# Performance work log

Hardware: AMD Instinct MI355X
Metric: run time of the kernel (lower is better)

The kernel has to match this reference:

```python
import jax, jax.numpy as jnp
import numpy as np

VOC_SIZE = 65536
DIM = 256
BATCH = 4096
NUM_TOPK = 32
TEMPERATURE = 1.0


def setup_inputs() -> dict:
    key = jax.random.key(0)
    ks = jax.random.split(key, 8)
    scale = 1.0 / np.sqrt(DIM)
    return {
        "x": jax.random.normal(ks[0], (BATCH, DIM), dtype=jnp.float32),
        "codebook": jax.random.normal(ks[1], (VOC_SIZE, DIM), dtype=jnp.float32),
        "Wq": jax.random.normal(ks[2], (DIM, DIM), dtype=jnp.float32) * scale,
        "bq": jax.random.normal(ks[3], (DIM,), dtype=jnp.float32) * scale,
        "Wk": jax.random.normal(ks[4], (DIM, DIM), dtype=jnp.float32) * scale,
        "bk": jax.random.normal(ks[5], (DIM,), dtype=jnp.float32) * scale,
        "Wv": jax.random.normal(ks[6], (DIM, DIM), dtype=jnp.float32) * scale,
        "bv": jax.random.normal(ks[7], (DIM,), dtype=jnp.float32) * scale,
    }


def reference(x, codebook, Wq, bq, Wk, bk, Wv, bv):
    # Linear projections (torch Linear: y = x @ W.T + b)
    q = x @ Wq.T + bq                      # [B, D]
    k = codebook @ Wk.T + bk               # [V, D]
    v = codebook @ Wv.T + bv               # [V, D]

    dots = jnp.einsum('bd,kd->bk', q, k)   # [B, V]
    top_value, top_ind = jax.lax.top_k(dots, NUM_TOPK)  # sorted desc, like torch.topk

    # mask everything strictly below the k-th largest score
    vk = top_value[:, -1:]                 # [B, 1]
    mask_value = -jnp.finfo(dots.dtype).max
    dots_masked = jnp.where(dots < vk, mask_value, dots)

    attn = jax.nn.softmax(dots_masked / TEMPERATURE, axis=-1)
    out = jnp.einsum('bk,kd->bd', attn, v)  # [B, D]
    return (out, top_value, top_ind, dots_masked)
```

## Files before the change

kernel.cpp:

```cpp
#include <hip/hip_runtime.h>
#include <float.h>
#include <math.h>

#define DIMK 256
#define VOC 65536
#define BATCH 4096
#define NTOP 32

#define MASKV -3.3895313892515355e+38f

typedef __bf16 bf16x8 __attribute__((ext_vector_type(8)));
typedef float f32x4 __attribute__((ext_vector_type(4)));
typedef float f4 __attribute__((ext_vector_type(4)));
typedef unsigned int u32x4 __attribute__((ext_vector_type(4)));
typedef unsigned int u32x2 __attribute__((ext_vector_type(2)));

__device__ __forceinline__ ushort f2bf(float f) {
    unsigned u = __float_as_uint(f);
    u = (u + 0x7fffu + ((u >> 16) & 1u)) >> 16;
    return (ushort)u;
}
__device__ __forceinline__ float bflo(unsigned u) { return __uint_as_float(u << 16); }
__device__ __forceinline__ float bfhi(unsigned u) { return __uint_as_float(u & 0xFFFF0000u); }

#define GLOAD_LDS16(gsrc, ldst)                                                \
    __builtin_amdgcn_global_load_lds(                                          \
        (const __attribute__((address_space(1))) unsigned int*)(gsrc),         \
        (__attribute__((address_space(3))) unsigned int*)(ldst), 16, 0, 0)

__global__ __launch_bounds__(256) void gemm_nt(
    const float* __restrict__ A, const float* __restrict__ B,
    const float* __restrict__ bias, float* __restrict__ C, int N, int swap, int obf16)
{
    __shared__ float As[16][132];
    __shared__ float Bs[16][132];
    const int bn = swap ? blockIdx.y : blockIdx.x;
    const int bm = swap ? blockIdx.x : blockIdx.y;
    const int tid = threadIdx.x;
    const int tx = tid & 15, ty = tid >> 4;
    const float* Ab = A + (size_t)bm * 128 * DIMK;
    const float* Bb = B + (size_t)bn * 128 * DIMK;

    float acc[2][2][4][4];
#pragma unroll
    for (int rg = 0; rg < 2; rg++)
#pragma unroll
        for (int cg = 0; cg < 2; cg++)
#pragma unroll
            for (int r = 0; r < 4; r++)
#pragma unroll
                for (int c = 0; c < 4; c++) acc[rg][cg][r][c] = 0.f;

    for (int k0 = 0; k0 < DIMK; k0 += 16) {
#pragma unroll
        for (int r = 0; r < 2; ++r) {
            int i = tid + r * 256;
            int row = i >> 2;
            int kc = (i & 3) << 2;
            const float4 va = *(const float4*)(Ab + (size_t)row * DIMK + k0 + kc);
            As[kc + 0][row] = va.x; As[kc + 1][row] = va.y;
            As[kc + 2][row] = va.z; As[kc + 3][row] = va.w;
            const float4 vb = *(const float4*)(Bb + (size_t)row * DIMK + k0 + kc);
            Bs[kc + 0][row] = vb.x; Bs[kc + 1][row] = vb.y;
            Bs[kc + 2][row] = vb.z; Bs[kc + 3][row] = vb.w;
        }
        __syncthreads();
#pragma unroll
        for (int k = 0; k < 16; ++k) {
            const float4 a0 = *(const float4*)&As[k][ty * 4];
            const float4 a1 = *(const float4*)&As[k][64 + ty * 4];
            const float4 b0 = *(const float4*)&Bs[k][tx * 4];
            const float4 b1 = *(const float4*)&Bs[k][64 + tx * 4];
            const float ar[2][4] = { {a0.x, a0.y, a0.z, a0.w}, {a1.x, a1.y, a1.z, a1.w} };
            const float bc[2][4] = { {b0.x, b0.y, b0.z, b0.w}, {b1.x, b1.y, b1.z, b1.w} };
#pragma unroll
            for (int rg = 0; rg < 2; rg++)
#pragma unroll
                for (int cg = 0; cg < 2; cg++)
#pragma unroll
                    for (int r = 0; r < 4; r++)
#pragma unroll
                        for (int c = 0; c < 4; c++)
                            acc[rg][cg][r][c] = fmaf(ar[rg][r], bc[cg][c], acc[rg][cg][r][c]);
        }
        __syncthreads();
    }

#pragma unroll
    for (int rg = 0; rg < 2; rg++)
#pragma unroll
        for (int r = 0; r < 4; r++) {
            size_t row = (size_t)bm * 128 + rg * 64 + ty * 4 + r;
#pragma unroll
            for (int cg = 0; cg < 2; cg++) {
                int col = bn * 128 + cg * 64 + tx * 4;
                float4 o;
                o.x = acc[rg][cg][r][0]; o.y = acc[rg][cg][r][1];
                o.z = acc[rg][cg][r][2]; o.w = acc[rg][cg][r][3];
                if (bias) {
                    o.x += bias[col + 0]; o.y += bias[col + 1];
                    o.z += bias[col + 2]; o.w += bias[col + 3];
                }
                if (obf16) {
                    ushort4 ob;
                    ob.x = f2bf(o.x); ob.y = f2bf(o.y);
                    ob.z = f2bf(o.z); ob.w = f2bf(o.w);
                    *(ushort4*)((ushort*)C + row * (size_t)N + col) = ob;
                } else {
                    *(float4*)(C + row * (size_t)N + col) = o;
                }
            }
        }
}

__global__ __launch_bounds__(256) void cast_f32_bf16(
    const float* __restrict__ src, ushort* __restrict__ dst, int n8)
{
    const int i = blockIdx.x * 256 + threadIdx.x;
    if (i >= n8) return;
    const f4 a = *(const f4*)(src + (size_t)i * 8);
    const f4 b = *(const f4*)(src + (size_t)i * 8 + 4);
    u32x4 o;
    o.x = (unsigned)f2bf(a.x) | ((unsigned)f2bf(a.y) << 16);
    o.y = (unsigned)f2bf(a.z) | ((unsigned)f2bf(a.w) << 16);
    o.z = (unsigned)f2bf(b.x) | ((unsigned)f2bf(b.y) << 16);
    o.w = (unsigned)f2bf(b.z) | ((unsigned)f2bf(b.w) << 16);
    *(u32x4*)(dst + (size_t)i * 8) = o;
}

__global__ __launch_bounds__(256) void gemm_bf16_nt(
    const ushort* __restrict__ Ab16, const ushort* __restrict__ Bb16,
    const float* __restrict__ bias, ushort* __restrict__ C, int ldc)
{
    __shared__ __align__(16) ushort As[2][128 * 32];
    __shared__ __align__(16) ushort Bs[2][128 * 32];
    const int bm = blockIdx.x;
    const int bn = blockIdx.y;
    const int tid = threadIdx.x;
    const int w = tid >> 6, l = tid & 63;
    const int wm = w >> 1, wn = w & 1;

    const ushort* Ab = Ab16 + (size_t)bm * 128 * DIMK;
    const ushort* Bb = Bb16 + (size_t)bn * 128 * DIMK;

    const int sr = l >> 2;
    const int sc = (l & 3) ^ ((l >> 3) & 3);
    const int fr = l & 15;
    const int pc = (l >> 4) ^ ((fr >> 1) & 3);

    const int slab0 = w * 2, slab1 = w * 2 + 1;
    const ushort* gA0 = Ab + (size_t)(slab0 * 16 + sr) * DIMK + sc * 8;
    const ushort* gA1 = Ab + (size_t)(slab1 * 16 + sr) * DIMK + sc * 8;
    const ushort* gB0 = Bb + (size_t)(slab0 * 16 + sr) * DIMK + sc * 8;
    const ushort* gB1 = Bb + (size_t)(slab1 * 16 + sr) * DIMK + sc * 8;

#define STAGE_G(buf, kk) do {                                    \
        GLOAD_LDS16(gA0 + (kk), &As[buf][slab0 * 512]);          \
        GLOAD_LDS16(gB0 + (kk), &Bs[buf][slab0 * 512]);          \
        GLOAD_LDS16(gA1 + (kk), &As[buf][slab1 * 512]);          \
        GLOAD_LDS16(gB1 + (kk), &Bs[buf][slab1 * 512]);          \
    } while (0)

    f32x4 acc[4][4];
    const f32x4 zero = {0.f, 0.f, 0.f, 0.f};
#pragma unroll
    for (int i = 0; i < 4; ++i)
#pragma unroll
        for (int j = 0; j < 4; ++j) acc[i][j] = zero;

    STAGE_G(0, 0);
    asm volatile("s_waitcnt vmcnt(0)" ::: "memory");
    __builtin_amdgcn_s_barrier();
    asm volatile("" ::: "memory");

#pragma unroll
    for (int t = 0; t < 8; ++t) {
        const int cur = t & 1;
        if (t < 7) STAGE_G(cur ^ 1, (t + 1) * 32);

        uint4 a4[4], b4[4];
#pragma unroll
        for (int f = 0; f < 4; ++f) {
            a4[f] = *(const uint4*)(&As[cur][(wm * 64 + f * 16 + fr) * 32 + pc * 8]);
            b4[f] = *(const uint4*)(&Bs[cur][(wn * 64 + f * 16 + fr) * 32 + pc * 8]);
        }
#pragma unroll
        for (int i = 0; i < 4; ++i)
#pragma unroll
            for (int j = 0; j < 4; ++j)
                acc[i][j] = __builtin_amdgcn_mfma_f32_16x16x32_bf16(
                    __builtin_bit_cast(bf16x8, b4[i]),
                    __builtin_bit_cast(bf16x8, a4[j]),
                    acc[i][j], 0, 0, 0);

        if (t < 7) {
            asm volatile("s_waitcnt vmcnt(0)" ::: "memory");
            __builtin_amdgcn_s_barrier();
            asm volatile("" ::: "memory");
        }
    }
#undef STAGE_G

    const int nq = (l >> 4) * 4;
    const int mc = l & 15;
#pragma unroll
    for (int i = 0; i < 4; ++i)
#pragma unroll
        for (int j = 0; j < 4; ++j) {
            const int n0 = bn * 128 + wn * 64 + i * 16 + nq;
            const size_t m = (size_t)(bm * 128 + wm * 64 + j * 16 + mc);
            const f4 bb = *(const f4*)(bias + n0);
            const float c0 = acc[i][j][0] + bb.x, c1 = acc[i][j][1] + bb.y;
            const float c2 = acc[i][j][2] + bb.z, c3 = acc[i][j][3] + bb.w;
            unsigned p0, p1;
            asm("v_cvt_pk_bf16_f32 %0, %1, %2" : "=v"(p0) : "v"(c0), "v"(c1));
            asm("v_cvt_pk_bf16_f32 %0, %1, %2" : "=v"(p1) : "v"(c2), "v"(c3));
            u32x2 pv; pv.x = p0; pv.y = p1;
            *(u32x2*)(C + m * (size_t)ldc + n0) = pv;
        }
}

__global__ __launch_bounds__(256) void dots_mfma(
    const ushort* __restrict__ Qb,
    const ushort* __restrict__ Kb,
    ushort* __restrict__ Db,
    float* __restrict__ Rm)
{
    __shared__ __align__(16) ushort As[2][128 * 32];
    __shared__ __align__(16) ushort Bs[2][128 * 32];
    const int bm = blockIdx.x;
    const int bn = blockIdx.y;
    const int tid = threadIdx.x;
    const int w = tid >> 6, l = tid & 63;
    const int wm = w >> 1, wn = w & 1;

    const ushort* Ab = Qb + (size_t)bm * 128 * DIMK;
    const ushort* Bb = Kb + (size_t)bn * 128 * DIMK;

    const int sr = l >> 2;
    const int sc = (l & 3) ^ ((l >> 3) & 3);
    const int fr = l & 15;
    const int pc = (l >> 4) ^ ((fr >> 1) & 3);

    const int slab0 = w * 2, slab1 = w * 2 + 1;
    const ushort* gA0 = Ab + (size_t)(slab0 * 16 + sr) * DIMK + sc * 8;
    const ushort* gA1 = Ab + (size_t)(slab1 * 16 + sr) * DIMK + sc * 8;
    const ushort* gB0 = Bb + (size_t)(slab0 * 16 + sr) * DIMK + sc * 8;
    const ushort* gB1 = Bb + (size_t)(slab1 * 16 + sr) * DIMK + sc * 8;

#define STAGE_DM(buf, kk) do {                                   \
        GLOAD_LDS16(gA0 + (kk), &As[buf][slab0 * 512]);          \
        GLOAD_LDS16(gB0 + (kk), &Bs[buf][slab0 * 512]);          \
        GLOAD_LDS16(gA1 + (kk), &As[buf][slab1 * 512]);          \
        GLOAD_LDS16(gB1 + (kk), &Bs[buf][slab1 * 512]);          \
    } while (0)

    f32x4 acc[4][4];
    const f32x4 zero = {0.f, 0.f, 0.f, 0.f};
#pragma unroll
    for (int i = 0; i < 4; ++i)
#pragma unroll
        for (int j = 0; j < 4; ++j) acc[i][j] = zero;

    STAGE_DM(0, 0);
    asm volatile("s_waitcnt vmcnt(0)" ::: "memory");
    __builtin_amdgcn_s_barrier();
    asm volatile("" ::: "memory");

#pragma unroll
    for (int t = 0; t < 8; ++t) {
        const int cur = t & 1;
        if (t < 7) STAGE_DM(cur ^ 1, (t + 1) * 32);

        uint4 a4[4], b4[4];
#pragma unroll
        for (int f = 0; f < 4; ++f) {
            a4[f] = *(const uint4*)(&As[cur][(wm * 64 + f * 16 + fr) * 32 + pc * 8]);
            b4[f] = *(const uint4*)(&Bs[cur][(wn * 64 + f * 16 + fr) * 32 + pc * 8]);
        }
#pragma unroll
        for (int i = 0; i < 4; ++i)
#pragma unroll
            for (int j = 0; j < 4; ++j)
                acc[i][j] = __builtin_amdgcn_mfma_f32_16x16x32_bf16(
                    __builtin_bit_cast(bf16x8, b4[i]),
                    __builtin_bit_cast(bf16x8, a4[j]),
                    acc[i][j], 0, 0, 0);

        if (t < 7) {
            asm volatile("s_waitcnt vmcnt(0)" ::: "memory");
            __builtin_amdgcn_s_barrier();
            asm volatile("" ::: "memory");
        }
    }
#undef STAGE_DM

    const int kq = (l >> 4) * 4;
    const int qc = l & 15;
#pragma unroll
    for (int i = 0; i < 4; ++i)
#pragma unroll
        for (int j = 0; j < 4; ++j) {
            const size_t q = (size_t)(bm * 128 + wm * 64 + j * 16 + qc);
            const size_t k = (size_t)(bn * 128 + wn * 64 + i * 16 + kq);
            unsigned p0, p1;
            asm("v_cvt_pk_bf16_f32 %0, %1, %2" : "=v"(p0) : "v"(acc[i][j][0]), "v"(acc[i][j][1]));
            asm("v_cvt_pk_bf16_f32 %0, %1, %2" : "=v"(p1) : "v"(acc[i][j][2]), "v"(acc[i][j][3]));
            u32x2 pv; pv.x = p0; pv.y = p1;
            *(u32x2*)(Db + q * (size_t)(2 * VOC) + k) = pv;
        }

#pragma unroll
    for (int j = 0; j < 4; ++j) {
        float m = -FLT_MAX;
#pragma unroll
        for (int i = 0; i < 4; ++i)
#pragma unroll
            for (int r = 0; r < 4; ++r) m = fmaxf(m, acc[i][j][r]);
        m = fmaxf(m, __shfl_xor(m, 16));
        m = fmaxf(m, __shfl_xor(m, 32));
        if (l < 16) {
            const size_t qrow = (size_t)(bm * 128 + wm * 64 + j * 16 + l);
            Rm[qrow * 1024 + (bn * 2 + wn)] = bflo((unsigned)f2bf(m));
        }
    }
}

__device__ __forceinline__ bool pair_gt(float av, int ai, float bv, int bi) {
    return (av > bv) || (av == bv && ai < bi);
}

__global__ __launch_bounds__(256) void row_tail(
    float* __restrict__ dots, const float* __restrict__ Rm,
    float* __restrict__ topv, int* __restrict__ topi,
    const float* __restrict__ codebook, const float* __restrict__ Wv,
    const float* __restrict__ bvec, float* __restrict__ out)
{
    const int row = blockIdx.x;
    const int tid = threadIdx.x;
    const int w = tid >> 6, l = tid & 63;
    float* rp = dots + ((size_t)row << 16);

    __shared__ float s_wt[4];
    __shared__ int   s_cnt;
    __shared__ float cv[1024];
    __shared__ int   ci[1024];
    __shared__ float s_t32v[NTOP];
    __shared__ int   s_t32i[NTOP];
    __shared__ float s_attn[NTOP];
    __shared__ float s_inv;
    __shared__ float s_wc[256];

    const f4 rv = *(const f4*)(Rm + (size_t)row * 1024 + tid * 4);
    const float tmax = fmaxf(fmaxf(rv.x, rv.y), fmaxf(rv.z, rv.w));

    float cur = tmax, Tw = -FLT_MAX;
#pragma unroll
    for (int r = 0; r < 8; ++r) {
        float m = cur;
#pragma unroll
        for (int off = 32; off; off >>= 1) m = fmaxf(m, __shfl_xor(m, off));
        Tw = m;
        cur = (cur == m) ? -FLT_MAX : cur;
    }
    if (l == 0) s_wt[w] = Tw;
    if (tid == 0) s_cnt = 0;
    __syncthreads();
    const float Tb = fminf(fminf(s_wt[0], s_wt[1]), fminf(s_wt[2], s_wt[3]));

    const u32x4* rb = (const u32x4*)rp;
#pragma unroll
    for (int c = 0; c < 4; ++c) {
        if (rv[c] >= Tb) {
            const int kt = tid * 4 + c;
#pragma unroll
            for (int g = 0; g < 8; ++g) {
                const u32x4 u = rb[kt * 8 + g];
                const float vv[8] = { bflo(u.x), bfhi(u.x), bflo(u.y), bfhi(u.y),
                                      bflo(u.z), bfhi(u.z), bflo(u.w), bfhi(u.w) };
#pragma unroll
                for (int j = 0; j < 8; ++j) {
                    if (vv[j] >= Tb) {
                        const int p = atomicAdd(&s_cnt, 1);
                        if (p < 1024) { cv[p] = vv[j]; ci[p] = kt * 64 + g * 8 + j; }
                    }
                }
            }
        }
    }
    __syncthreads();
    const int n = (s_cnt < 1024) ? s_cnt : 1024;

    if (w == 0) {
        for (int r = 0; r < NTOP; ++r) {
            float bv_ = -FLT_MAX; int bi_ = 0x7fffffff;
            for (int p = l; p < n; p += 64) {
                const float vv = cv[p]; const int ii = ci[p];
                if (pair_gt(vv, ii, bv_, bi_)) { bv_ = vv; bi_ = ii; }
            }
#pragma unroll
            for (int off = 32; off; off >>= 1) {
                const float ov = __shfl_xor(bv_, off);
                const int   oi = __shfl_xor(bi_, off);
                if (pair_gt(ov, oi, bv_, bi_)) { bv_ = ov; bi_ = oi; }
            }
            if (l == 0) {
                topv[(size_t)row * NTOP + r] = bv_;
                topi[(size_t)row * NTOP + r] = bi_;
                s_t32v[r] = bv_; s_t32i[r] = bi_;
            }
            for (int p = l; p < n; p += 64)
                if (ci[p] == bi_) { cv[p] = -FLT_MAX; ci[p] = 0x7fffffff; }
        }
    }

    {
        const f4 mv4 = { MASKV, MASKV, MASKV, MASKV };
        f4* rp4 = (f4*)rp;
        const int base = w * (VOC / 4 / 4);
        for (int c4 = base + l; c4 < base + VOC / 4 / 4; c4 += 64)
            __builtin_nontemporal_store(mv4, rp4 + c4);
    }
    __syncthreads();
    if (tid < NTOP) rp[s_t32i[tid]] = s_t32v[tid];

    if (tid < NTOP) s_attn[tid] = expf(s_t32v[tid] - s_t32v[0]);
    __syncthreads();
    if (tid == 0) {
        float s = 0.f;
        for (int j = 0; j < NTOP; j++) s += s_attn[j];
        s_inv = 1.0f / s;
    }
    __syncthreads();

    float wc = 0.f;
    for (int j = 0; j < NTOP; j++)
        wc = fmaf(s_attn[j], codebook[(size_t)s_t32i[j] * DIMK + tid], wc);
    wc *= s_inv;

    s_wc[tid] = wc;
    __syncthreads();

    float acc = bvec[tid];
    const float4* wr = (const float4*)(Wv + (size_t)tid * DIMK);
#pragma unroll 4
    for (int e = 0; e < DIMK / 4; e++) {
        float4 wv4 = wr[e];
        acc = fmaf(wv4.x, s_wc[4 * e + 0], acc);
        acc = fmaf(wv4.y, s_wc[4 * e + 1], acc);
        acc = fmaf(wv4.z, s_wc[4 * e + 2], acc);
        acc = fmaf(wv4.w, s_wc[4 * e + 3], acc);
    }
    out[(size_t)row * DIMK + tid] = acc;
}

extern "C" void kernel_launch(void* const* d_in, const int* in_sizes, int n_in,
                              void* d_out, int out_size, void* d_ws, size_t ws_size,
                              hipStream_t stream) {
    const float* x        = (const float*)d_in[0];
    const float* codebook = (const float*)d_in[1];
    const float* Wq       = (const float*)d_in[2];
    const float* bq       = (const float*)d_in[3];
    const float* Wk       = (const float*)d_in[4];
    const float* bk       = (const float*)d_in[5];
    const float* Wv       = (const float*)d_in[6];
    const float* bv       = (const float*)d_in[7];

    float* out_f = (float*)d_out;
    float* topv  = out_f + (size_t)BATCH * DIMK;
    int*   topi  = (int*)(topv + (size_t)BATCH * NTOP);
    float* dotsm = (float*)(topi + (size_t)BATCH * NTOP);

    ushort* kb16 = (ushort*)d_ws;
    ushort* qb16 = kb16 + (size_t)VOC * DIMK;
    float*  Rm   = (float*)(qb16 + (size_t)BATCH * DIMK);

    ushort* cb16  = (ushort*)dotsm;
    ushort* wkb16 = cb16 + (size_t)VOC * DIMK;

    cast_f32_bf16<<<VOC * DIMK / 8 / 256, 256, 0, stream>>>(codebook, cb16, VOC * DIMK / 8);
    cast_f32_bf16<<<DIMK * DIMK / 8 / 256, 256, 0, stream>>>(Wk, wkb16, DIMK * DIMK / 8);
    gemm_nt<<<dim3(DIMK / 128, BATCH / 128), 256, 0, stream>>>(x, Wq, bq, (float*)qb16, DIMK, 0, 1);
    gemm_bf16_nt<<<dim3(VOC / 128, DIMK / 128), 256, 0, stream>>>(cb16, wkb16, bk, kb16, DIMK);
    dots_mfma<<<dim3(BATCH / 128, VOC / 128), 256, 0, stream>>>(qb16, kb16, (ushort*)dotsm, Rm);
    row_tail<<<BATCH, 256, 0, stream>>>(dotsm, Rm, topv, topi, codebook, Wv, bv, out_f);
}
```

Baseline: 1.619 ms.

## Split row tail into select, grid-wide mask fill, and attention kernels

Breaks the per-row tail kernel into three launches. The first scans the bf16 dots and selects the top-k per row, the second does a grid-strided nontemporal fill of the whole masked dots buffer, and the third writes back the top-k values and computes the attention output. Previously the fill ran inside the same block as the serial single-wave top-k selection, so the other waves idled and the store bandwidth was tied to row scheduling. The split costs two extra launches and an extra round trip of topv/topi through global memory.

```diff
diff --git a/kernel.cpp b/kernel.cpp
--- a/kernel.cpp
+++ b/kernel.cpp
@@ -330,26 +330,18 @@
     return (av > bv) || (av == bv && ai < bi);
 }
 
-__global__ __launch_bounds__(256) void row_tail(
-    float* __restrict__ dots, const float* __restrict__ Rm,
-    float* __restrict__ topv, int* __restrict__ topi,
-    const float* __restrict__ codebook, const float* __restrict__ Wv,
-    const float* __restrict__ bvec, float* __restrict__ out)
+__global__ __launch_bounds__(256) void scan_select(
+    const float* __restrict__ dots, const float* __restrict__ Rm,
+    float* __restrict__ topv, int* __restrict__ topi)
 {
     const int row = blockIdx.x;
     const int tid = threadIdx.x;
     const int w = tid >> 6, l = tid & 63;
-    float* rp = dots + ((size_t)row << 16);
 
     __shared__ float s_wt[4];
     __shared__ int   s_cnt;
     __shared__ float cv[1024];
     __shared__ int   ci[1024];
-    __shared__ float s_t32v[NTOP];
-    __shared__ int   s_t32i[NTOP];
-    __shared__ float s_attn[NTOP];
-    __shared__ float s_inv;
-    __shared__ float s_wc[256];
 
     const f4 rv = *(const f4*)(Rm + (size_t)row * 1024 + tid * 4);
     const float tmax = fmaxf(fmaxf(rv.x, rv.y), fmaxf(rv.z, rv.w));
@@ -368,7 +360,7 @@
     __syncthreads();
     const float Tb = fminf(fminf(s_wt[0], s_wt[1]), fminf(s_wt[2], s_wt[3]));
 
-    const u32x4* rb = (const u32x4*)rp;
+    const u32x4* rb = (const u32x4*)(dots + ((size_t)row << 16));
 #pragma unroll
     for (int c = 0; c < 4; ++c) {
         if (rv[c] >= Tb) {
@@ -391,38 +383,61 @@
     __syncthreads();
     const int n = (s_cnt < 1024) ? s_cnt : 1024;
 
-    if (w == 0) {
-        for (int r = 0; r < NTOP; ++r) {
-            float bv_ = -FLT_MAX; int bi_ = 0x7fffffff;
-            for (int p = l; p < n; p += 64) {
-                const float vv = cv[p]; const int ii = ci[p];
-                if (pair_gt(vv, ii, bv_, bi_)) { bv_ = vv; bi_ = ii; }
-            }
-#pragma unroll
-            for (int off = 32; off; off >>= 1) {
-                const float ov = __shfl_xor(bv_, off);
-                const int   oi = __shfl_xor(bi_, off);
-                if (pair_gt(ov, oi, bv_, bi_)) { bv_ = ov; bi_ = oi; }
-            }
-            if (l == 0) {
-                topv[(size_t)row * NTOP + r] = bv_;
-                topi[(size_t)row * NTOP + r] = bi_;
-                s_t32v[r] = bv_; s_t32i[r] = bi_;
-            }
-            for (int p = l; p < n; p += 64)
-                if (ci[p] == bi_) { cv[p] = -FLT_MAX; ci[p] = 0x7fffffff; }
-        }
-    }
-
-    {
-        const f4 mv4 = { MASKV, MASKV, MASKV, MASKV };
-        f4* rp4 = (f4*)rp;
-        const int base = w * (VOC / 4 / 4);
-        for (int c4 = base + l; c4 < base + VOC / 4 / 4; c4 += 64)
-            __builtin_nontemporal_store(mv4, rp4 + c4);
+    if (w != 0) return;
+
+    for (int r = 0; r < NTOP; ++r) {
+        float bv_ = -FLT_MAX; int bi_ = 0x7fffffff;
+        for (int p = l; p < n; p += 64) {
+            const float vv = cv[p]; const int ii = ci[p];
+            if (pair_gt(vv, ii, bv_, bi_)) { bv_ = vv; bi_ = ii; }
+        }
+#pragma unroll
+        for (int off = 32; off; off >>= 1) {
+            const float ov = __shfl_xor(bv_, off);
+            const int   oi = __shfl_xor(bi_, off);
+            if (pair_gt(ov, oi, bv_, bi_)) { bv_ = ov; bi_ = oi; }
+        }
+        if (l == 0) {
+            topv[(size_t)row * NTOP + r] = bv_;
+            topi[(size_t)row * NTOP + r] = bi_;
+        }
+        for (int p = l; p < n; p += 64)
+            if (ci[p] == bi_) { cv[p] = -FLT_MAX; ci[p] = 0x7fffffff; }
+    }
+}
+
+__global__ __launch_bounds__(256) void fill_all(float* __restrict__ dots)
+{
+    const f4 mv4 = { MASKV, MASKV, MASKV, MASKV };
+    f4* p = (f4*)dots;
+    const size_t n = (size_t)BATCH * VOC / 4;
+    const size_t stride = (size_t)gridDim.x * 256;
+    for (size_t i = (size_t)blockIdx.x * 256 + threadIdx.x; i < n; i += stride)
+        __builtin_nontemporal_store(mv4, p + i);
+}
+
+__global__ __launch_bounds__(256) void tail_k(
+    float* __restrict__ dots, const float* __restrict__ topv, const int* __restrict__ topi,
+    const float* __restrict__ codebook, const float* __restrict__ Wv,
+    const float* __restrict__ bvec, float* __restrict__ out)
+{
+    const int row = blockIdx.x;
+    const int tid = threadIdx.x;
+    float* rp = dots + ((size_t)row << 16);
+
+    __shared__ float s_t32v[NTOP];
+    __shared__ int   s_t32i[NTOP];
+    __shared__ float s_attn[NTOP];
+    __shared__ float s_inv;
+    __shared__ float s_wc[256];
+
+    if (tid < NTOP) {
+        const float tv = topv[(size_t)row * NTOP + tid];
+        const int   ti = topi[(size_t)row * NTOP + tid];
+        s_t32v[tid] = tv; s_t32i[tid] = ti;
+        rp[ti] = tv;
     }
     __syncthreads();
-    if (tid < NTOP) rp[s_t32i[tid]] = s_t32v[tid];
 
     if (tid < NTOP) s_attn[tid] = expf(s_t32v[tid] - s_t32v[0]);
     __syncthreads();
@@ -483,5 +498,7 @@
     gemm_nt<<<dim3(DIMK / 128, BATCH / 128), 256, 0, stream>>>(x, Wq, bq, (float*)qb16, DIMK, 0, 1);
     gemm_bf16_nt<<<dim3(VOC / 128, DIMK / 128), 256, 0, stream>>>(cb16, wkb16, bk, kb16, DIMK);
     dots_mfma<<<dim3(BATCH / 128, VOC / 128), 256, 0, stream>>>(qb16, kb16, (ushort*)dotsm, Rm);
-    row_tail<<<BATCH, 256, 0, stream>>>(dotsm, Rm, topv, topi, codebook, Wv, bv, out_f);
-}
+    scan_select<<<BATCH, 256, 0, stream>>>(dotsm, Rm, topv, topi);
+    fill_all<<<2048, 256, 0, stream>>>(dotsm);
+    tail_k<<<BATCH, 256, 0, stream>>>(dotsm, topv, topi, codebook, Wv, bv, out_f);
+}
```

After: 1.748 ms. 7.9% more time.
